# Kernel tuning notes

Measured on AMD Instinct MI355X. Metric: run time of the kernel, lower is better.

Reference implementation:

```python
import jax, jax.numpy as jnp
import numpy as np

IN_F, OUT_F, N_CH, N_TILES, PTS = 256, 256, 1024, 1024, 256
OMEGA = 30.0


def setup_inputs() -> dict:
    key = jax.random.key(0)
    kx, kw, kb, ki = jax.random.split(key, 4)
    bound = float(np.sqrt(6.0 / IN_F) / OMEGA)  # SIREN-style init (is_first=False)
    x = jax.random.normal(kx, (N_TILES, PTS, IN_F), dtype=jnp.float32)
    weight = jax.random.uniform(kw, (N_CH, IN_F, OUT_F), dtype=jnp.float32,
                                minval=-bound, maxval=bound)
    bias = jax.random.uniform(kb, (1, 1, OUT_F), dtype=jnp.float32,
                              minval=-bound, maxval=bound)
    indices = jax.random.randint(ki, (N_TILES,), 0, N_CH, dtype=jnp.int64)
    return {"x": x, "weight": weight, "bias": bias, "indices": indices}


def reference(x, weight, bias, indices):
    # gather per-tile weight slice then batched matmul: [T,P,I] @ [T,I,O] -> [T,P,O]
    w = weight[indices]                      # [T, I, O]
    out = jnp.einsum('tpi,tio->tpo', x, w) + bias[0]
    return jnp.sin(OMEGA * out)
```

## Files before the change

### kernel.cpp

```cpp
#include <hip/hip_runtime.h>

typedef _Float16 half8_t __attribute__((ext_vector_type(8)));
typedef _Float16 half4_t __attribute__((ext_vector_type(4)));
typedef float    float4_t __attribute__((ext_vector_type(4)));

#define N_TILES 1024
#define PTS     256
#define IN_F    256
#define OUT_F   256
#define BM      128
#define BK      32
#define LDK     40
#define NSTEP   (IN_F / BK)
#define OMEGA_C 30.0f

__global__ __launch_bounds__(512, 4)
void siren_tile_gemm(const float* __restrict__ x,
                     const float* __restrict__ w,
                     const float* __restrict__ bias,
                     const void* __restrict__ idx_raw,
                     float* __restrict__ out) {
  __shared__ __align__(16) _Float16 Al[2][BM][LDK];
  __shared__ __align__(16) _Float16 Bl[2][OUT_F][LDK];

  const int tid = threadIdx.x;

  const int s_id = blockIdx.x;
  const int xcd  = s_id & 7;
  const int k_id = s_id >> 3;
  const int tile = xcd + 8 * (k_id >> 1);
  const int mh   = k_id & 1;

  const int hiw  = ((const int*)idx_raw)[2 * (tid & 63) + 1];
  const bool is32 = __any(hiw != 0);
  const int ch = is32 ? ((const int*)idx_raw)[tile]
                      : (int)(((const long long*)idx_raw)[tile]);

  const float* __restrict__ Xg = x + (size_t)tile * (PTS * IN_F) + (size_t)mh * BM * IN_F;
  const float* __restrict__ Wg = w + (size_t)ch * (IN_F * OUT_F);
  float*       __restrict__ Og = out + (size_t)tile * (PTS * OUT_F) + (size_t)mh * BM * OUT_F;

  const int a_row = tid >> 3;
  const int a_lir = tid & 7;
  const int b_kb  = tid >> 6;
  const int b_nb  = tid & 63;

  float4_t acc[4][4];
#pragma unroll
  for (int m = 0; m < 4; ++m)
#pragma unroll
    for (int n = 0; n < 4; ++n)
      acc[m][n] = (float4_t){0.f, 0.f, 0.f, 0.f};

  float4_t a_ld[2], b_ld[4];

#define BSWZ(g, n) (((g) ^ (((n) >> 3) & 3)))

#pragma unroll
  for (int p = 0; p < 2; ++p)
    a_ld[p] = *(const float4_t*)(Xg + (size_t)(a_row + 64 * p) * IN_F + a_lir * 4);
#pragma unroll
  for (int j = 0; j < 4; ++j)
    b_ld[j] = *(const float4_t*)(Wg + (size_t)(b_kb * 4 + j) * OUT_F + b_nb * 4);
#pragma unroll
  for (int p = 0; p < 2; ++p) {
    half4_t h = {(_Float16)a_ld[p].x, (_Float16)a_ld[p].y,
                 (_Float16)a_ld[p].z, (_Float16)a_ld[p].w};
    *(half4_t*)&Al[0][a_row + 64 * p][a_lir * 4] = h;
  }
#pragma unroll
  for (int i = 0; i < 4; ++i) {
    const int n = b_nb * 4 + i;
    half4_t h = {(_Float16)b_ld[0][i], (_Float16)b_ld[1][i],
                 (_Float16)b_ld[2][i], (_Float16)b_ld[3][i]};
    *(half4_t*)&Bl[0][n][BSWZ(b_kb >> 1, n) * 8 + (b_kb & 1) * 4] = h;
  }
  __syncthreads();

  const int lane = tid & 63;
  const int wid  = tid >> 6;
  const int wm   = (wid >> 2) * 64;
  const int wn   = (wid & 3) * 64;
  const int fr   = lane & 15;
  const int kg   = lane >> 4;

#pragma unroll 2
  for (int s = 0; s < NSTEP; ++s) {
    const int cur = s & 1;
    if (s + 1 < NSTEP) {
      const int k0 = (s + 1) * BK;
#pragma unroll
      for (int p = 0; p < 2; ++p)
        a_ld[p] = *(const float4_t*)(Xg + (size_t)(a_row + 64 * p) * IN_F + k0 + a_lir * 4);
    }

    half8_t af[4], bf[4];
#pragma unroll
    for (int m = 0; m < 4; ++m)
      af[m] = *(const half8_t*)&Al[cur][wm + m * 16 + fr][kg * 8];
#pragma unroll
    for (int n = 0; n < 4; ++n) {
      const int r = wn + n * 16 + fr;
      bf[n] = *(const half8_t*)&Bl[cur][r][BSWZ(kg, r) * 8];
    }

#pragma unroll
    for (int m = 0; m < 4; ++m)
#pragma unroll
      for (int n = 0; n < 4; ++n)
        acc[m][n] = __builtin_amdgcn_mfma_f32_16x16x32_f16(af[m], bf[n], acc[m][n], 0, 0, 0);

    __builtin_amdgcn_sched_barrier(0);

    if (s + 1 < NSTEP) {
      const int k0 = (s + 1) * BK;
      const int nxt = cur ^ 1;
#pragma unroll
      for (int j = 0; j < 4; ++j)
        b_ld[j] = *(const float4_t*)(Wg + (size_t)(k0 + b_kb * 4 + j) * OUT_F + b_nb * 4);
#pragma unroll
      for (int p = 0; p < 2; ++p) {
        half4_t h = {(_Float16)a_ld[p].x, (_Float16)a_ld[p].y,
                     (_Float16)a_ld[p].z, (_Float16)a_ld[p].w};
        *(half4_t*)&Al[nxt][a_row + 64 * p][a_lir * 4] = h;
      }
#pragma unroll
      for (int i = 0; i < 4; ++i) {
        const int n = b_nb * 4 + i;
        half4_t h = {(_Float16)b_ld[0][i], (_Float16)b_ld[1][i],
                     (_Float16)b_ld[2][i], (_Float16)b_ld[3][i]};
        *(half4_t*)&Bl[nxt][n][BSWZ(b_kb >> 1, n) * 8 + (b_kb & 1) * 4] = h;
      }
      __syncthreads();
    }
  }

  float bv[4];
#pragma unroll
  for (int n = 0; n < 4; ++n) bv[n] = OMEGA_C * bias[wn + n * 16 + fr];

#pragma unroll
  for (int m = 0; m < 4; ++m) {
#pragma unroll
    for (int n = 0; n < 4; ++n) {
#pragma unroll
      for (int j = 0; j < 4; ++j) {
        const int row = wm + m * 16 + kg * 4 + j;
        const int col = wn + n * 16 + fr;
        Og[(size_t)row * OUT_F + col] = __sinf(fmaf(OMEGA_C, acc[m][n][j], bv[n]));
      }
    }
  }
}

extern "C" void kernel_launch(void* const* d_in, const int* in_sizes, int n_in,
                              void* d_out, int out_size, void* d_ws, size_t ws_size,
                              hipStream_t stream) {
  const float* x    = (const float*)d_in[0];
  const float* w    = (const float*)d_in[1];
  const float* bias = (const float*)d_in[2];
  const void*  idx  = d_in[3];
  float*       out  = (float*)d_out;

  siren_tile_gemm<<<N_TILES * 2, 512, 0, stream>>>(x, w, bias, idx, out);
}
```

Before: 160.0 us.

## Halve M tile, double grid, and prefetch global loads two steps ahead

Cuts the per-block M tile from 128 to 64 rows, so the grid has four blocks per tile instead of two, giving more blocks for latency hiding. Global loads are now issued two k-steps ahead into a register double buffer, with a manual barrier that waits only on lgkmcnt. The sched_barrier is removed and the k-loop is fully unrolled. In exchange, each W slice is loaded twice as many times, which raises L2 and HBM traffic for the weights, and register pressure goes up from the extra staged loads.

```diff
diff --git a/kernel.cpp b/kernel.cpp
--- a/kernel.cpp
+++ b/kernel.cpp
@@ -8,11 +8,19 @@
 #define PTS     256
 #define IN_F    256
 #define OUT_F   256
-#define BM      128
+#define BM      64
 #define BK      32
 #define LDK     40
 #define NSTEP   (IN_F / BK)
 #define OMEGA_C 30.0f
+
+#define BARRIER() do {                                        \
+    asm volatile("s_waitcnt lgkmcnt(0)" ::: "memory");        \
+    __builtin_amdgcn_s_barrier();                             \
+    asm volatile("" ::: "memory");                            \
+  } while (0)
+
+#define BSWZ(g, n) (((g) ^ (((n) >> 3) & 3)))
 
 __global__ __launch_bounds__(512, 4)
 void siren_tile_gemm(const float* __restrict__ x,
@@ -25,78 +33,78 @@
 
   const int tid = threadIdx.x;
 
-  const int s_id = blockIdx.x;
-  const int xcd  = s_id & 7;
-  const int k_id = s_id >> 3;
-  const int tile = xcd + 8 * (k_id >> 1);
-  const int mh   = k_id & 1;
+  const int b    = blockIdx.x;
+  const int xcd  = b & 7;
+  const int rest = b >> 3;
+  const int tile = xcd + 8 * (rest >> 2);
+  const int mq   = rest & 3;
 
   const int hiw  = ((const int*)idx_raw)[2 * (tid & 63) + 1];
   const bool is32 = __any(hiw != 0);
   const int ch = is32 ? ((const int*)idx_raw)[tile]
                       : (int)(((const long long*)idx_raw)[tile]);
 
-  const float* __restrict__ Xg = x + (size_t)tile * (PTS * IN_F) + (size_t)mh * BM * IN_F;
+  const float* __restrict__ Xg = x + (size_t)tile * (PTS * IN_F) + (size_t)mq * BM * IN_F;
   const float* __restrict__ Wg = w + (size_t)ch * (IN_F * OUT_F);
-  float*       __restrict__ Og = out + (size_t)tile * (PTS * OUT_F) + (size_t)mh * BM * OUT_F;
+  float*       __restrict__ Og = out + (size_t)tile * (PTS * OUT_F) + (size_t)mq * BM * OUT_F;
 
   const int a_row = tid >> 3;
-  const int a_lir = tid & 7;
+  const int a_col = (tid & 7) * 4;
   const int b_kb  = tid >> 6;
   const int b_nb  = tid & 63;
 
-  float4_t acc[4][4];
+  float4_t acc[2][4];
 #pragma unroll
-  for (int m = 0; m < 4; ++m)
+  for (int m = 0; m < 2; ++m)
 #pragma unroll
     for (int n = 0; n < 4; ++n)
       acc[m][n] = (float4_t){0.f, 0.f, 0.f, 0.f};
 
-  float4_t a_ld[2], b_ld[4];
+  float4_t aS[2];
+  float4_t bS[2][4];
 
-#define BSWZ(g, n) (((g) ^ (((n) >> 3) & 3)))
+#define ISSUE(slot, s)                                                          \
+  do {                                                                          \
+    const int k0_ = (s) * BK;                                                   \
+    aS[slot] = *(const float4_t*)(Xg + (size_t)a_row * IN_F + k0_ + a_col);     \
+    _Pragma("unroll")                                                           \
+    for (int j = 0; j < 4; ++j)                                                 \
+      bS[slot][j] = *(const float4_t*)(Wg + (size_t)(k0_ + b_kb * 4 + j) * OUT_F + b_nb * 4); \
+  } while (0)
 
-#pragma unroll
-  for (int p = 0; p < 2; ++p)
-    a_ld[p] = *(const float4_t*)(Xg + (size_t)(a_row + 64 * p) * IN_F + a_lir * 4);
-#pragma unroll
-  for (int j = 0; j < 4; ++j)
-    b_ld[j] = *(const float4_t*)(Wg + (size_t)(b_kb * 4 + j) * OUT_F + b_nb * 4);
-#pragma unroll
-  for (int p = 0; p < 2; ++p) {
-    half4_t h = {(_Float16)a_ld[p].x, (_Float16)a_ld[p].y,
-                 (_Float16)a_ld[p].z, (_Float16)a_ld[p].w};
-    *(half4_t*)&Al[0][a_row + 64 * p][a_lir * 4] = h;
-  }
-#pragma unroll
-  for (int i = 0; i < 4; ++i) {
-    const int n = b_nb * 4 + i;
-    half4_t h = {(_Float16)b_ld[0][i], (_Float16)b_ld[1][i],
-                 (_Float16)b_ld[2][i], (_Float16)b_ld[3][i]};
-    *(half4_t*)&Bl[0][n][BSWZ(b_kb >> 1, n) * 8 + (b_kb & 1) * 4] = h;
-  }
-  __syncthreads();
+#define STORE_LDS(slot, buf)                                                    \
+  do {                                                                          \
+    half4_t ha_ = {(_Float16)aS[slot].x, (_Float16)aS[slot].y,                  \
+                   (_Float16)aS[slot].z, (_Float16)aS[slot].w};                 \
+    *(half4_t*)&Al[buf][a_row][a_col] = ha_;                                    \
+    _Pragma("unroll")                                                           \
+    for (int i = 0; i < 4; ++i) {                                               \
+      const int n_ = b_nb * 4 + i;                                              \
+      half4_t hb_ = {(_Float16)bS[slot][0][i], (_Float16)bS[slot][1][i],        \
+                     (_Float16)bS[slot][2][i], (_Float16)bS[slot][3][i]};       \
+      *(half4_t*)&Bl[buf][n_][BSWZ(b_kb >> 1, n_) * 8 + (b_kb & 1) * 4] = hb_;  \
+    }                                                                           \
+  } while (0)
+
+  ISSUE(0, 0);
+  ISSUE(1, 1);
+  STORE_LDS(0, 0);
+  BARRIER();
 
   const int lane = tid & 63;
   const int wid  = tid >> 6;
-  const int wm   = (wid >> 2) * 64;
+  const int wm   = (wid >> 2) * 32;
   const int wn   = (wid & 3) * 64;
   const int fr   = lane & 15;
   const int kg   = lane >> 4;
 
-#pragma unroll 2
+#pragma unroll
   for (int s = 0; s < NSTEP; ++s) {
     const int cur = s & 1;
-    if (s + 1 < NSTEP) {
-      const int k0 = (s + 1) * BK;
+
+    half8_t af[2], bf[4];
 #pragma unroll
-      for (int p = 0; p < 2; ++p)
-        a_ld[p] = *(const float4_t*)(Xg + (size_t)(a_row + 64 * p) * IN_F + k0 + a_lir * 4);
-    }
-
-    half8_t af[4], bf[4];
-#pragma unroll
-    for (int m = 0; m < 4; ++m)
+    for (int m = 0; m < 2; ++m)
       af[m] = *(const half8_t*)&Al[cur][wm + m * 16 + fr][kg * 8];
 #pragma unroll
     for (int n = 0; n < 4; ++n) {
@@ -105,33 +113,15 @@
     }
 
 #pragma unroll
-    for (int m = 0; m < 4; ++m)
+    for (int m = 0; m < 2; ++m)
 #pragma unroll
       for (int n = 0; n < 4; ++n)
         acc[m][n] = __builtin_amdgcn_mfma_f32_16x16x32_f16(af[m], bf[n], acc[m][n], 0, 0, 0);
 
-    __builtin_amdgcn_sched_barrier(0);
-
+    if (s + 2 < NSTEP) ISSUE(cur, s + 2);
     if (s + 1 < NSTEP) {
-      const int k0 = (s + 1) * BK;
-      const int nxt = cur ^ 1;
-#pragma unroll
-      for (int j = 0; j < 4; ++j)
-        b_ld[j] = *(const float4_t*)(Wg + (size_t)(k0 + b_kb * 4 + j) * OUT_F + b_nb * 4);
-#pragma unroll
-      for (int p = 0; p < 2; ++p) {
-        half4_t h = {(_Float16)a_ld[p].x, (_Float16)a_ld[p].y,
-                     (_Float16)a_ld[p].z, (_Float16)a_ld[p].w};
-        *(half4_t*)&Al[nxt][a_row + 64 * p][a_lir * 4] = h;
-      }
-#pragma unroll
-      for (int i = 0; i < 4; ++i) {
-        const int n = b_nb * 4 + i;
-        half4_t h = {(_Float16)b_ld[0][i], (_Float16)b_ld[1][i],
-                     (_Float16)b_ld[2][i], (_Float16)b_ld[3][i]};
-        *(half4_t*)&Bl[nxt][n][BSWZ(b_kb >> 1, n) * 8 + (b_kb & 1) * 4] = h;
-      }
-      __syncthreads();
+      STORE_LDS(cur ^ 1, cur ^ 1);
+      BARRIER();
     }
   }
 
@@ -140,7 +130,7 @@
   for (int n = 0; n < 4; ++n) bv[n] = OMEGA_C * bias[wn + n * 16 + fr];
 
 #pragma unroll
-  for (int m = 0; m < 4; ++m) {
+  for (int m = 0; m < 2; ++m) {
 #pragma unroll
     for (int n = 0; n < 4; ++n) {
 #pragma unroll
@@ -162,5 +152,5 @@
   const void*  idx  = d_in[3];
   float*       out  = (float*)d_out;
 
-  siren_tile_gemm<<<N_TILES * 2, 512, 0, stream>>>(x, w, bias, idx, out);
+  siren_tile_gemm<<<N_TILES * 4, 512, 0, stream>>>(x, w, bias, idx, out);
 }
```

Result: slower. 166.2 us (+3.9%).

## Split tiles along output columns, stage full-K weight slice in LDS, stream X to registers

Applied to the files above, without the earlier changes.

Each block now covers all 256 rows of a tile and half of the output columns, instead of half the rows and all columns. The block loads its whole 256x128 weight slice into LDS once as fp16 with an XOR swizzle, behind a single barrier. X fragments are read straight from global memory into registers, converted to fp16 in registers, and prefetched one K-step ahead. This removes the per-step double-buffered LDS staging and the seven per-iteration barriers. The costs are that the MFMA loop cannot start until the whole weight slice is loaded, uncoalesced direct X loads, 64 KB of LDS per block that may limit occupancy, and X being read twice per tile instead of W.

```diff
diff --git a/kernel.cpp b/kernel.cpp
--- a/kernel.cpp
+++ b/kernel.cpp
@@ -8,11 +8,15 @@
 #define PTS     256
 #define IN_F    256
 #define OUT_F   256
-#define BM      128
-#define BK      32
-#define LDK     40
-#define NSTEP   (IN_F / BK)
+#define BN      128
+#define NSTEP   8
 #define OMEGA_C 30.0f
+
+#define BARRIER() do {                                        \
+    asm volatile("s_waitcnt lgkmcnt(0)" ::: "memory");        \
+    __builtin_amdgcn_s_barrier();                             \
+    asm volatile("" ::: "memory");                            \
+  } while (0)
 
 __global__ __launch_bounds__(512, 4)
 void siren_tile_gemm(const float* __restrict__ x,
@@ -20,30 +24,62 @@
                      const float* __restrict__ bias,
                      const void* __restrict__ idx_raw,
                      float* __restrict__ out) {
-  __shared__ __align__(16) _Float16 Al[2][BM][LDK];
-  __shared__ __align__(16) _Float16 Bl[2][OUT_F][LDK];
+  __shared__ _Float16 Wl[BN * 256];
 
   const int tid = threadIdx.x;
 
-  const int s_id = blockIdx.x;
-  const int xcd  = s_id & 7;
-  const int k_id = s_id >> 3;
-  const int tile = xcd + 8 * (k_id >> 1);
-  const int mh   = k_id & 1;
+  const int b    = blockIdx.x;
+  const int xcd  = b & 7;
+  const int rest = b >> 3;
+  const int tile = xcd + 8 * (rest >> 1);
+  const int nh   = rest & 1;
 
   const int hiw  = ((const int*)idx_raw)[2 * (tid & 63) + 1];
   const bool is32 = __any(hiw != 0);
   const int ch = is32 ? ((const int*)idx_raw)[tile]
                       : (int)(((const long long*)idx_raw)[tile]);
 
-  const float* __restrict__ Xg = x + (size_t)tile * (PTS * IN_F) + (size_t)mh * BM * IN_F;
-  const float* __restrict__ Wg = w + (size_t)ch * (IN_F * OUT_F);
-  float*       __restrict__ Og = out + (size_t)tile * (PTS * OUT_F) + (size_t)mh * BM * OUT_F;
+  const float* __restrict__ Xg = x + (size_t)tile * (PTS * IN_F);
+  const float* __restrict__ Wg = w + (size_t)ch * (IN_F * OUT_F) + nh * BN;
+  float*       __restrict__ Og = out + (size_t)tile * (PTS * OUT_F) + nh * BN;
 
-  const int a_row = tid >> 3;
-  const int a_lir = tid & 7;
-  const int b_kb  = tid >> 6;
-  const int b_nb  = tid & 63;
+  const int lane = tid & 63;
+  const int wid  = tid >> 6;
+  const int wm   = (wid >> 1) * 64;
+  const int wn   = (wid & 1) * 64;
+  const int fr   = lane & 15;
+  const int kg   = lane >> 4;
+
+  float4_t xa[8];
+#pragma unroll
+  for (int m = 0; m < 4; ++m)
+#pragma unroll
+    for (int h = 0; h < 2; ++h)
+      xa[m * 2 + h] = *(const float4_t*)(Xg + (size_t)(wm + m * 16 + fr) * IN_F + kg * 8 + h * 4);
+
+  {
+    const int s8o = tid >> 8;
+    const int kb  = (tid >> 5) & 7;
+    const int nb  = tid & 31;
+#pragma unroll
+    for (int sp = 0; sp < 4; ++sp) {
+      const int s8 = sp * 2 + s8o;
+      const int k0 = s8 * 32 + kb * 4;
+      float4_t wv[4];
+#pragma unroll
+      for (int j = 0; j < 4; ++j)
+        wv[j] = *(const float4_t*)(Wg + (size_t)(k0 + j) * OUT_F + nb * 4);
+#pragma unroll
+      for (int i = 0; i < 4; ++i) {
+        const int n = nb * 4 + i;
+        const int g = s8 * 4 + (kb >> 1);
+        half4_t hb = {(_Float16)wv[0][i], (_Float16)wv[1][i],
+                      (_Float16)wv[2][i], (_Float16)wv[3][i]};
+        *(half4_t*)&Wl[n * 256 + (g ^ (n & 7)) * 8 + (kb & 1) * 4] = hb;
+      }
+    }
+  }
+  BARRIER();
 
   float4_t acc[4][4];
 #pragma unroll
@@ -52,56 +88,30 @@
     for (int n = 0; n < 4; ++n)
       acc[m][n] = (float4_t){0.f, 0.f, 0.f, 0.f};
 
-  float4_t a_ld[2], b_ld[4];
-
-#define BSWZ(g, n) (((g) ^ (((n) >> 3) & 3)))
-
 #pragma unroll
-  for (int p = 0; p < 2; ++p)
-    a_ld[p] = *(const float4_t*)(Xg + (size_t)(a_row + 64 * p) * IN_F + a_lir * 4);
+  for (int s = 0; s < NSTEP; ++s) {
+    half8_t af[4];
 #pragma unroll
-  for (int j = 0; j < 4; ++j)
-    b_ld[j] = *(const float4_t*)(Wg + (size_t)(b_kb * 4 + j) * OUT_F + b_nb * 4);
+    for (int m = 0; m < 4; ++m) {
+      const float4_t lo = xa[m * 2], hi = xa[m * 2 + 1];
+      af[m] = (half8_t){(_Float16)lo.x, (_Float16)lo.y, (_Float16)lo.z, (_Float16)lo.w,
+                        (_Float16)hi.x, (_Float16)hi.y, (_Float16)hi.z, (_Float16)hi.w};
+    }
+    if (s + 1 < NSTEP) {
+      const int k0 = (s + 1) * 32;
 #pragma unroll
-  for (int p = 0; p < 2; ++p) {
-    half4_t h = {(_Float16)a_ld[p].x, (_Float16)a_ld[p].y,
-                 (_Float16)a_ld[p].z, (_Float16)a_ld[p].w};
-    *(half4_t*)&Al[0][a_row + 64 * p][a_lir * 4] = h;
-  }
+      for (int m = 0; m < 4; ++m)
 #pragma unroll
-  for (int i = 0; i < 4; ++i) {
-    const int n = b_nb * 4 + i;
-    half4_t h = {(_Float16)b_ld[0][i], (_Float16)b_ld[1][i],
-                 (_Float16)b_ld[2][i], (_Float16)b_ld[3][i]};
-    *(half4_t*)&Bl[0][n][BSWZ(b_kb >> 1, n) * 8 + (b_kb & 1) * 4] = h;
-  }
-  __syncthreads();
-
-  const int lane = tid & 63;
-  const int wid  = tid >> 6;
-  const int wm   = (wid >> 2) * 64;
-  const int wn   = (wid & 3) * 64;
-  const int fr   = lane & 15;
-  const int kg   = lane >> 4;
-
-#pragma unroll 2
-  for (int s = 0; s < NSTEP; ++s) {
-    const int cur = s & 1;
-    if (s + 1 < NSTEP) {
-      const int k0 = (s + 1) * BK;
-#pragma unroll
-      for (int p = 0; p < 2; ++p)
-        a_ld[p] = *(const float4_t*)(Xg + (size_t)(a_row + 64 * p) * IN_F + k0 + a_lir * 4);
+        for (int h = 0; h < 2; ++h)
+          xa[m * 2 + h] = *(const float4_t*)(Xg + (size_t)(wm + m * 16 + fr) * IN_F + k0 + kg * 8 + h * 4);
     }
 
-    half8_t af[4], bf[4];
-#pragma unroll
-    for (int m = 0; m < 4; ++m)
-      af[m] = *(const half8_t*)&Al[cur][wm + m * 16 + fr][kg * 8];
+    half8_t bf[4];
 #pragma unroll
     for (int n = 0; n < 4; ++n) {
       const int r = wn + n * 16 + fr;
-      bf[n] = *(const half8_t*)&Bl[cur][r][BSWZ(kg, r) * 8];
+      const int g = s * 4 + kg;
+      bf[n] = *(const half8_t*)&Wl[r * 256 + (g ^ (r & 7)) * 8];
     }
 
 #pragma unroll
@@ -109,35 +119,11 @@
 #pragma unroll
       for (int n = 0; n < 4; ++n)
         acc[m][n] = __builtin_amdgcn_mfma_f32_16x16x32_f16(af[m], bf[n], acc[m][n], 0, 0, 0);
-
-    __builtin_amdgcn_sched_barrier(0);
-
-    if (s + 1 < NSTEP) {
-      const int k0 = (s + 1) * BK;
-      const int nxt = cur ^ 1;
-#pragma unroll
-      for (int j = 0; j < 4; ++j)
-        b_ld[j] = *(const float4_t*)(Wg + (size_t)(k0 + b_kb * 4 + j) * OUT_F + b_nb * 4);
-#pragma unroll
-      for (int p = 0; p < 2; ++p) {
-        half4_t h = {(_Float16)a_ld[p].x, (_Float16)a_ld[p].y,
-                     (_Float16)a_ld[p].z, (_Float16)a_ld[p].w};
-        *(half4_t*)&Al[nxt][a_row + 64 * p][a_lir * 4] = h;
-      }
-#pragma unroll
-      for (int i = 0; i < 4; ++i) {
-        const int n = b_nb * 4 + i;
-        half4_t h = {(_Float16)b_ld[0][i], (_Float16)b_ld[1][i],
-                     (_Float16)b_ld[2][i], (_Float16)b_ld[3][i]};
-        *(half4_t*)&Bl[nxt][n][BSWZ(b_kb >> 1, n) * 8 + (b_kb & 1) * 4] = h;
-      }
-      __syncthreads();
-    }
   }
 
   float bv[4];
 #pragma unroll
-  for (int n = 0; n < 4; ++n) bv[n] = OMEGA_C * bias[wn + n * 16 + fr];
+  for (int n = 0; n < 4; ++n) bv[n] = OMEGA_C * bias[nh * BN + wn + n * 16 + fr];
 
 #pragma unroll
   for (int m = 0; m < 4; ++m) {
```

Result: slower. 206.2 us (+28.9%).
